# Kernel tuning notes

Measured on AMD Instinct MI355X. Metric: run time of the kernel, lower is better.

## Reference

```python
import jax, jax.numpy as jnp
import numpy as np

DIM, HEADS, WS = 192, 8, 8
B, H, W = 4, 256, 256


def conv2d(x, w, b=None, padding=((0, 0), (0, 0)), groups=1):
    y = jax.lax.conv_general_dilated(
        x, w, window_strides=(1, 1), padding=padding,
        dimension_numbers=("NCHW", "OIHW", "NCHW"), feature_group_count=groups)
    if b is not None:
        y = y + b[None, :, None, None]
    return y


def setup_inputs() -> dict:
    key = jax.random.key(0)
    ks = jax.random.split(key, 16)
    d = DIM
    s = 0.02
    return {
        "x": jax.random.normal(ks[0], (B, d, H, W), jnp.float32),
        "w_dww": jax.random.normal(ks[1], (d, 1, 1, 11), jnp.float32) * s,
        "b_dww": jnp.zeros((d,), jnp.float32),
        "w_dwh": jax.random.normal(ks[2], (d, 1, 11, 1), jnp.float32) * s,
        "b_dwh": jnp.zeros((d,), jnp.float32),
        "w_dwhw": jax.random.normal(ks[3], (2 * d, 1, 3, 3), jnp.float32) * s,
        "b_dwhw": jnp.zeros((2 * d,), jnp.float32),
        "w_conv1": jax.random.normal(ks[4], (d, 2 * d, 1, 1), jnp.float32) * s,
        "w_qkv": jax.random.normal(ks[5], (3 * d, d, 1, 1), jnp.float32) * s,
        "w_qkvdw": jax.random.normal(ks[6], (3 * d, 1, 3, 3), jnp.float32) * s,
        "w_conv2": jax.random.normal(ks[7], (d, d, 1, 1), jnp.float32) * s,
        "w_conv3": jax.random.normal(ks[8], (d, d, 1, 1), jnp.float32) * s,
        "w_conv4a": jax.random.normal(ks[9], (d, d, 1, 1), jnp.float32) * s,
        "w_conv4b": jax.random.normal(ks[10], (d, 1, 3, 3), jnp.float32) * s,
        "w_proj": jax.random.normal(ks[11], (d, 2 * d, 1, 1), jnp.float32) * s,
        "temperature": jnp.ones((HEADS, 1, 1), jnp.float32),
    }


def reference(x, w_dww, b_dww, w_dwh, b_dwh, w_dwhw, b_dwhw, w_conv1,
              w_qkv, w_qkvdw, w_conv2, w_conv3, w_conv4a, w_conv4b,
              w_proj, temperature):
    b, c, h, w = x.shape
    d, heads, ws = DIM, HEADS, WS

    # high-frequency branch: strip depthwise convs -> 3x3 depthwise -> 1x1
    hw_cat = jnp.concatenate([
        conv2d(x, w_dww, b_dww, padding=((0, 0), (5, 5)), groups=d),
        conv2d(x, w_dwh, b_dwh, padding=((5, 5), (0, 0)), groups=d)], axis=1)
    high = conv2d(hw_cat, w_dwhw, b_dwhw, padding=((1, 1), (1, 1)), groups=2 * d)
    high = conv2d(high, w_conv1)  # [b, d, h, w]

    # low-frequency branch: avg-pool downsample then channel attention
    x_down = x.reshape(b, c, h // ws, ws, w // ws, ws).mean(axis=(3, 5))
    qkv = conv2d(x_down, w_qkv)
    qkv = conv2d(qkv, w_qkvdw, padding=((1, 1), (1, 1)), groups=3 * d)
    q, k, v = jnp.split(qkv, 3, axis=1)

    hd, wd = h // ws, w // ws
    ch = d // heads
    q = q.reshape(b, heads, ch, hd * wd)
    k = k.reshape(b, heads, ch, hd * wd)
    q = q / jnp.maximum(jnp.linalg.norm(q, axis=-1, keepdims=True), 1e-12)
    k = k / jnp.maximum(jnp.linalg.norm(k, axis=-1, keepdims=True), 1e-12)
    attn = jnp.einsum("bhcn,bhdn->bhcd", q, k) * temperature[None]  # [b,heads,ch,ch]
    attn = jax.nn.softmax(attn, axis=-1)

    # pooling gate on v (global 1x1) then modulate full-res conv4(x)
    v_max = jnp.max(v, axis=(2, 3), keepdims=True)
    v_avg = jnp.mean(v, axis=(2, 3), keepdims=True)
    v_gate = conv2d(v_max, w_conv2) + conv2d(v_avg, w_conv3)  # [b, d, 1, 1]
    x4 = conv2d(conv2d(x, w_conv4a), w_conv4b, padding=((1, 1), (1, 1)), groups=d)
    v_full = v_gate * x4  # [b, d, h, w]

    v_full = v_full.reshape(b, heads, ch, h * w)
    low = jnp.einsum("bhcd,bhdn->bhcn", attn, v_full).reshape(b, d, h, w)

    return conv2d(jnp.concatenate([high, low], axis=1), w_proj)
```

## Files before the change

### kernel.cpp

```cpp
#include <hip/hip_runtime.h>
#include <hip/hip_bf16.h>

typedef __hip_bfloat16 bf16;
typedef __attribute__((ext_vector_type(8))) short s8v;
typedef __attribute__((ext_vector_type(4))) float f4;
typedef __attribute__((ext_vector_type(2))) float f2;

#define DEVI __device__ __forceinline__

DEVI f4 mfma16(s8v a, s8v b, f4 c){
  return __builtin_amdgcn_mfma_f32_16x16x32_bf16(a, b, c, 0, 0, 0);
}

constexpr int NPIX = 65536;
constexpr int NDOWN = 1024;

__global__ void k_cast_w(const float* __restrict__ w1, const float* __restrict__ w4a,
                         const float* __restrict__ wp, const float* __restrict__ wq,
                         bf16* __restrict__ out){
  int i = blockIdx.x*256 + threadIdx.x;
  if (i < 73728) out[i] = __float2bfloat16(w1[i]);
  else if (i < 110592) out[i] = __float2bfloat16(w4a[i - 73728]);
  else if (i < 184320) out[i] = __float2bfloat16(wp[i - 110592]);
  else if (i < 294912) out[i] = __float2bfloat16(wq[i - 184320]);
}

__global__ void k_pack_x(const float* __restrict__ x, bf16* __restrict__ xp){
  __shared__ float t[8][1032];
  int b = blockIdx.z, cb = blockIdx.y, ns = blockIdx.x, tid = threadIdx.x;
  const float* src = x + ((size_t)(b*192 + cb*8))*NPIX + ns*1024;
  #pragma unroll
  for (int i = 0; i < 8; ++i){
    float4 v = *(const float4*)(src + (size_t)i*NPIX + tid*4);
    *(float4*)&t[i][tid*4] = v;
  }
  __syncthreads();
  bf16* dst = xp + (((size_t)(b*24 + cb))*NPIX + ns*1024)*8;
  #pragma unroll
  for (int j = 0; j < 4; ++j){
    int p = j*256 + tid;
    alignas(16) bf16 c8[8];
    #pragma unroll
    for (int i = 0; i < 8; ++i) c8[i] = __float2bfloat16(t[i][p]);
    *(uint4*)(dst + (size_t)p*8) = *(const uint4*)c8;
  }
}

__global__ void k_pool(const bf16* __restrict__ xp, bf16* __restrict__ xdp){
  __shared__ float red[8][32][8];
  int b = blockIdx.z, cb = blockIdx.y, hd = blockIdx.x, tid = threadIdx.x;
  int r = tid >> 5, wd = tid & 31;
  const bf16* src = xp + (((size_t)(b*24 + cb))*NPIX + (hd*8 + r)*256 + wd*8)*8;
  float acc[8] = {0,0,0,0,0,0,0,0};
  #pragma unroll
  for (int ww = 0; ww < 8; ++ww){
    uint4 raw = *(const uint4*)(src + ww*8);
    const bf16* c8 = (const bf16*)&raw;
    #pragma unroll
    for (int i = 0; i < 8; ++i) acc[i] += __bfloat162float(c8[i]);
  }
  #pragma unroll
  for (int i = 0; i < 8; ++i) red[r][wd][i] = acc[i];
  __syncthreads();
  if (tid < 32){
    alignas(16) bf16 o8[8];
    #pragma unroll
    for (int i = 0; i < 8; ++i){
      float s = 0.f;
      #pragma unroll
      for (int rr = 0; rr < 8; ++rr) s += red[rr][tid][i];
      o8[i] = __float2bfloat16(s * (1.0f/64.0f));
    }
    *(uint4*)(xdp + (((size_t)(b*24 + cb))*NDOWN + hd*32 + tid)*8) = *(const uint4*)o8;
  }
}

template<int K, bool PLANAR>
__launch_bounds__(256, 2)
__global__ void k_gemm(const bf16* __restrict__ Bp, const bf16* __restrict__ W,
                       void* __restrict__ outp, int npix, int outkb){
  constexpr int KB8 = K/8;
  constexpr int NIT = K/64;
  __shared__ bf16 As[96*72];
  __shared__ bf16 Bs[128*72];
  int tid = threadIdx.x;
  int b = blockIdx.z;
  int m0 = blockIdx.y*96;
  int n0 = blockIdx.x*128;
  int wave = tid >> 6, lane = tid & 63;
  int wm = wave >> 1, wn = wave & 1;
  int lr = lane & 15, kg = lane >> 4;
  f4 acc[3][4] = {};
  const size_t bK = (size_t)b * KB8;
  for (int kt = 0; kt < NIT; ++kt){
    {
      int idx = tid;
      #pragma unroll
      for (int j = 0; j < 3; ++j, idx += 256){
        int m = idx >> 3, kc = idx & 7;
        *(uint4*)&As[m*72 + kc*8] = *(const uint4*)(W + (size_t)(m0 + m)*K + kt*64 + kc*8);
      }
      idx = tid;
      #pragma unroll
      for (int j = 0; j < 4; ++j, idx += 256){
        int kb = idx >> 7, n = idx & 127;
        *(uint4*)&Bs[n*72 + kb*8] = *(const uint4*)(Bp + ((bK + kt*8 + kb)*npix + n0 + n)*8);
      }
    }
    __syncthreads();
    #pragma unroll
    for (int kk = 0; kk < 2; ++kk){
      s8v af[3]; s8v bfr[4];
      int ko = kk*32 + kg*8;
      #pragma unroll
      for (int mf = 0; mf < 3; ++mf) af[mf] = *(const s8v*)&As[(wm*48 + mf*16 + lr)*72 + ko];
      #pragma unroll
      for (int nf = 0; nf < 4; ++nf) bfr[nf] = *(const s8v*)&Bs[(wn*64 + nf*16 + lr)*72 + ko];
      #pragma unroll
      for (int mf = 0; mf < 3; ++mf)
        #pragma unroll
        for (int nf = 0; nf < 4; ++nf)
          acc[mf][nf] = mfma16(af[mf], bfr[nf], acc[mf][nf]);
    }
    __syncthreads();
  }
  int quad = lane >> 4;
  #pragma unroll
  for (int mf = 0; mf < 3; ++mf){
    int mb = m0 + wm*48 + mf*16 + quad*4;
    #pragma unroll
    for (int nf = 0; nf < 4; ++nf){
      int n = n0 + wn*64 + nf*16 + lr;
      if constexpr (PLANAR){
        float* o = (float*)outp;
        #pragma unroll
        for (int r2 = 0; r2 < 4; ++r2)
          o[((size_t)(b*outkb + mb + r2))*npix + n] = acc[mf][nf][r2];
      } else {
        bf16* o = (bf16*)outp;
        alignas(8) bf16 v4[4];
        #pragma unroll
        for (int r2 = 0; r2 < 4; ++r2) v4[r2] = __float2bfloat16(acc[mf][nf][r2]);
        *(uint2*)(o + ((size_t)(b*outkb + (mb >> 3))*npix + n)*8 + (mb & 7)) = *(const uint2*)v4;
      }
    }
  }
}

__launch_bounds__(256, 4)
__global__ void k_high_dw(const bf16* __restrict__ xp,
    const float* __restrict__ wdww, const float* __restrict__ bdww,
    const float* __restrict__ wdwh, const float* __restrict__ bdwh,
    const float* __restrict__ w3, const float* __restrict__ b3,
    bf16* __restrict__ hw3p){
  __shared__ bf16 xs[28*29*8];
  __shared__ float dws[2*8*364];
  int t = blockIdx.x, cb = blockIdx.y, b = blockIdx.z, tid = threadIdx.x;
  int r0 = (t >> 4)*16, c0 = (t & 15)*16;

  const bf16* src = xp + ((size_t)(b*24 + cb))*NPIX*8;
  for (int i = tid; i < 784; i += 256){
    int r = i/28, c = i - r*28;
    int gr = r0 + r - 6, gc = c0 + c - 6;
    uint4 v = {0,0,0,0};
    if ((unsigned)gr < 256u && (unsigned)gc < 256u)
      v = *(const uint4*)(src + ((size_t)(gr*256 + gc))*8);
    *(uint4*)&xs[(r*29 + c)*8] = v;
  }
  __syncthreads();

  auto strip_task = [&](int task, bool isH){
    int ch = task & 7, idx = task >> 3;
    int cg = cb*8 + ch;
    const float* wsrc = isH ? (wdww + cg*11) : (wdwh + cg*11);
    float wv[11];
    #pragma unroll
    for (int j = 0; j < 11; ++j) wv[j] = wsrc[j];
    float bias = isH ? bdww[cg] : bdwh[cg];
    int base = isH ? ((idx + 5)*29)*8 + ch : (idx + 5)*8 + ch;
    int istr = isH ? 8 : 29*8;
    float vbuf[28];
    #pragma unroll
    for (int i = 0; i < 28; ++i)
      vbuf[i] = __bfloat162float(xs[base + i*istr]);
    int fixedv = (isH ? r0 : c0) + idx - 1;
    int varb   = (isH ? c0 : r0) - 1;
    bool fok = (unsigned)fixedv < 256u;
    float out[18];
    #pragma unroll
    for (int i = 0; i < 18; ++i){
      float s = bias;
      #pragma unroll
      for (int j = 0; j < 11; ++j) s += wv[j]*vbuf[i + j];
      bool ok = fok && ((unsigned)(varb + i) < 256u);
      out[i] = ok ? s : 0.f;
    }
    if (isH){
      float* ob = &dws[ch*364 + idx*20];
      #pragma unroll
      for (int q = 0; q < 4; ++q){
        f4 v; v[0] = out[q*4]; v[1] = out[q*4+1]; v[2] = out[q*4+2]; v[3] = out[q*4+3];
        *(f4*)(ob + q*4) = v;
      }
      f2 v2; v2[0] = out[16]; v2[1] = out[17];
      *(f2*)(ob + 16) = v2;
    } else {
      float* ob = &dws[(8 + ch)*364 + idx];
      #pragma unroll
      for (int i = 0; i < 18; ++i) ob[i*20] = out[i];
    }
  };
  {
    bool isH = tid < 144;
    int task = isH ? tid : tid - 144;
    strip_task(task, isH);
    if (tid >= 224) strip_task(tid - 112, false);
  }
  __syncthreads();

  {
    int branch = tid >> 7, rr = (tid >> 3) & 15, ch = tid & 7;
    int cg = cb*8 + ch;
    const float* wsrc = w3 + (branch*192 + cg)*9;
    float w[9];
    #pragma unroll
    for (int k = 0; k < 9; ++k) w[k] = wsrc[k];
    float bias = b3[branch*192 + cg];
    float acc[16];
    #pragma unroll
    for (int i = 0; i < 16; ++i) acc[i] = bias;
    const float* plane = &dws[(branch*8 + ch)*364];
    #pragma unroll
    for (int dr = 0; dr < 3; ++dr){
      const float* rp = plane + (rr + dr)*20;
      float rowv[18];
      #pragma unroll
      for (int q = 0; q < 4; ++q){
        f4 v = *(const f4*)(rp + q*4);
        rowv[q*4] = v[0]; rowv[q*4+1] = v[1]; rowv[q*4+2] = v[2]; rowv[q*4+3] = v[3];
      }
      {
        f2 v2 = *(const f2*)(rp + 16);
        rowv[16] = v2[0]; rowv[17] = v2[1];
      }
      #pragma unroll
      for (int dc = 0; dc < 3; ++dc){
        float wv = w[dr*3 + dc];
        #pragma unroll
        for (int i = 0; i < 16; ++i) acc[i] += wv * rowv[i + dc];
      }
    }
    bf16* o = hw3p + (((size_t)(b*48 + branch*24 + cb))*NPIX + (size_t)(r0 + rr)*256 + c0)*8 + ch;
    #pragma unroll
    for (int i = 0; i < 16; ++i) o[i*8] = __float2bfloat16(acc[i]);
  }
}

__global__ void k_qkv_dw(const bf16* __restrict__ qkv0p, const float* __restrict__ wdw,
                         float* __restrict__ qkvd, float* __restrict__ vmax, float* __restrict__ vavg){
  __shared__ bf16 xs[34*34*8];
  __shared__ float red[256*8];
  int cb = blockIdx.x, b = blockIdx.y, tid = threadIdx.x;
  for (int i = tid; i < 1156; i += 256){
    int r = i/34, c = i - r*34;
    int gr = r - 1, gc = c - 1;
    uint4 v = {0,0,0,0};
    if ((unsigned)gr < 32u && (unsigned)gc < 32u)
      v = *(const uint4*)(qkv0p + (((size_t)(b*72 + cb))*NDOWN + gr*32 + gc)*8);
    *(uint4*)&xs[i*8] = v;
  }
  __syncthreads();
  float mxv[8], smv[8];
  #pragma unroll
  for (int ch = 0; ch < 8; ++ch){ mxv[ch] = -3.4e38f; smv[ch] = 0.f; }
  for (int j = 0; j < 4; ++j){
    int p = j*256 + tid;
    int r = p >> 5, c = p & 31;
    #pragma unroll
    for (int ch = 0; ch < 8; ++ch){
      float s = 0.f;
      #pragma unroll
      for (int dr = 0; dr < 3; ++dr)
        #pragma unroll
        for (int dc = 0; dc < 3; ++dc)
          s += wdw[(cb*8 + ch)*9 + dr*3 + dc] *
               __bfloat162float(xs[((r + dr)*34 + c + dc)*8 + ch]);
      qkvd[((size_t)(b*576 + cb*8 + ch))*NDOWN + p] = s;
      mxv[ch] = fmaxf(mxv[ch], s);
      smv[ch] += s;
    }
  }
  if (cb >= 48){
    #pragma unroll
    for (int ch = 0; ch < 8; ++ch) red[tid*8 + ch] = mxv[ch];
    __syncthreads();
    for (int st = 128; st > 0; st >>= 1){
      if (tid < st)
        #pragma unroll
        for (int ch = 0; ch < 8; ++ch)
          red[tid*8 + ch] = fmaxf(red[tid*8 + ch], red[(tid + st)*8 + ch]);
      __syncthreads();
    }
    if (tid < 8) vmax[b*192 + (cb - 48)*8 + tid] = red[tid];
    __syncthreads();
    #pragma unroll
    for (int ch = 0; ch < 8; ++ch) red[tid*8 + ch] = smv[ch];
    __syncthreads();
    for (int st = 128; st > 0; st >>= 1){
      if (tid < st)
        #pragma unroll
        for (int ch = 0; ch < 8; ++ch) red[tid*8 + ch] += red[(tid + st)*8 + ch];
      __syncthreads();
    }
    if (tid < 8) vavg[b*192 + (cb - 48)*8 + tid] = red[tid] * (1.0f/1024.0f);
  }
}

__global__ void k_attn(const float* __restrict__ qkvd, const float* __restrict__ temp,
                       float* __restrict__ attn){
  __shared__ float inv[48];
  __shared__ float sm[576];
  int bh = blockIdx.x;
  int b = bh >> 3, h = bh & 7;
  const float* qb = qkvd + ((size_t)(b*576 + h*24))*NDOWN;
  const float* kb = qkvd + ((size_t)(b*576 + 192 + h*24))*NDOWN;
  int tid = threadIdx.x, wave = tid >> 6, lane = tid & 63;
  for (int v = wave; v < 48; v += 4){
    const float* p = (v < 24) ? (qb + v*NDOWN) : (kb + (v - 24)*NDOWN);
    float s = 0.f;
    for (int i = lane; i < NDOWN; i += 64){ float xv = p[i]; s += xv*xv; }
    #pragma unroll
    for (int o = 32; o > 0; o >>= 1) s += __shfl_down(s, o);
    if (lane == 0) inv[v] = 1.0f / fmaxf(sqrtf(s), 1e-12f);
  }
  __syncthreads();
  float tp = temp[h];
  for (int pr = tid; pr < 576; pr += 256){
    int c = pr/24, d = pr - c*24;
    const float4* qp = (const float4*)(qb + c*NDOWN);
    const float4* kp = (const float4*)(kb + d*NDOWN);
    float s = 0.f;
    for (int i = 0; i < 256; ++i){
      float4 a = qp[i], e = kp[i];
      s += a.x*e.x + a.y*e.y + a.z*e.z + a.w*e.w;
    }
    sm[pr] = s * inv[c] * inv[24 + d] * tp;
  }
  __syncthreads();
  if (tid < 24){
    float mx = -3.4e38f;
    for (int d = 0; d < 24; ++d) mx = fmaxf(mx, sm[tid*24 + d]);
    float sum = 0.f;
    for (int d = 0; d < 24; ++d) sum += __expf(sm[tid*24 + d] - mx);
    float isum = 1.0f / sum;
    for (int d = 0; d < 24; ++d)
      attn[((size_t)bh)*576 + tid*24 + d] = __expf(sm[tid*24 + d] - mx) * isum;
  }
}

__global__ void k_gate(const float* __restrict__ vmax, const float* __restrict__ vavg,
                       const float* __restrict__ w2, const float* __restrict__ w3,
                       float* __restrict__ gate){
  __shared__ float vm[192], va[192];
  int b = blockIdx.x, tid = threadIdx.x;
  if (tid < 192){ vm[tid] = vmax[b*192 + tid]; va[tid] = vavg[b*192 + tid]; }
  __syncthreads();
  if (tid < 192){
    float s = 0.f;
    const float* w2r = w2 + tid*192;
    const float* w3r = w3 + tid*192;
    for (int k = 0; k < 192; ++k) s += w2r[k]*vm[k] + w3r[k]*va[k];
    gate[b*192 + tid] = s;
  }
}

__global__ void k_low(const bf16* __restrict__ x4ap, const float* __restrict__ attn,
                      const float* __restrict__ gate, const float* __restrict__ w4b,
                      bf16* __restrict__ hlp){
  __shared__ bf16 xt[3*18*18*10];
  __shared__ float a2[576];
  __shared__ float wt[216];
  __shared__ float vt[24*256];
  int t = blockIdx.x, h = blockIdx.y, b = blockIdx.z, tid = threadIdx.x;
  int r0 = (t >> 4)*16, c0 = (t & 15)*16;
  int ch0 = h*24;
  for (int i = tid; i < 576; i += 256)
    a2[i] = attn[((size_t)(b*8 + h))*576 + i] * gate[b*192 + ch0 + (i % 24)];
  for (int i = tid; i < 216; i += 256) wt[i] = w4b[ch0*9 + i];
  for (int i = tid; i < 972; i += 256){
    int kb = i/324, p = i - kb*324;
    int r = p/18, c = p - r*18;
    int gr = r0 + r - 1, gc = c0 + c - 1;
    uint4 v = {0,0,0,0};
    if ((unsigned)gr < 256u && (unsigned)gc < 256u)
      v = *(const uint4*)(x4ap + (((size_t)(b*24 + h*3 + kb))*NPIX + gr*256 + gc)*8);
    const unsigned* u = (const unsigned*)&v;
    #pragma unroll
    for (int k = 0; k < 4; ++k) *(unsigned*)&xt[i*10 + k*2] = u[k];
  }
  __syncthreads();
  {
    int r = tid >> 4, c = tid & 15;
    #pragma unroll
    for (int ch = 0; ch < 24; ++ch){
      int kb = ch >> 3, ci = ch & 7;
      float s = 0.f;
      #pragma unroll
      for (int dr = 0; dr < 3; ++dr)
        #pragma unroll
        for (int dc = 0; dc < 3; ++dc)
          s += wt[ch*9 + dr*3 + dc] *
               __bfloat162float(xt[((kb*18 + r + dr)*18 + c + dc)*10 + ci]);
      vt[ch*256 + tid] = s;
    }
  }
  __syncthreads();
  {
    float o[24];
    #pragma unroll
    for (int cc = 0; cc < 24; ++cc){
      float s = 0.f;
      #pragma unroll
      for (int d = 0; d < 24; ++d) s += a2[cc*24 + d] * vt[d*256 + tid];
      o[cc] = s;
    }
    int n = (r0 + (tid >> 4))*256 + c0 + (tid & 15);
    #pragma unroll
    for (int kb = 0; kb < 3; ++kb){
      alignas(16) bf16 c8[8];
      #pragma unroll
      for (int i = 0; i < 8; ++i) c8[i] = __float2bfloat16(o[kb*8 + i]);
      *(uint4*)(hlp + (((size_t)(b*48 + 24 + h*3 + kb))*NPIX + n)*8) = *(const uint4*)c8;
    }
  }
}

extern "C" void kernel_launch(void* const* d_in, const int* in_sizes, int n_in,
                              void* d_out, int out_size, void* d_ws, size_t ws_size,
                              hipStream_t stream){
  const float* x        = (const float*)d_in[0];
  const float* w_dww    = (const float*)d_in[1];
  const float* b_dww    = (const float*)d_in[2];
  const float* w_dwh    = (const float*)d_in[3];
  const float* b_dwh    = (const float*)d_in[4];
  const float* w_dwhw   = (const float*)d_in[5];
  const float* b_dwhw   = (const float*)d_in[6];
  const float* w_conv1  = (const float*)d_in[7];
  const float* w_qkv    = (const float*)d_in[8];
  const float* w_qkvdw  = (const float*)d_in[9];
  const float* w_conv2  = (const float*)d_in[10];
  const float* w_conv3  = (const float*)d_in[11];
  const float* w_conv4a = (const float*)d_in[12];
  const float* w_conv4b = (const float*)d_in[13];
  const float* w_proj   = (const float*)d_in[14];
  const float* temp     = (const float*)d_in[15];

  char* ws = (char*)d_ws;
  size_t off = 0;
  auto take = [&](size_t bytes)->char*{
    char* r = ws + off;
    off = (off + bytes + 255) & ~(size_t)255;
    return r;
  };
  bf16*  xp    = (bf16*) take((size_t)4*192*65536*2);
  bf16*  hw3p  = (bf16*) take((size_t)4*384*65536*2);
  bf16*  hlp   = (bf16*) take((size_t)4*384*65536*2);
  bf16*  x4ap  = (bf16*) take((size_t)4*192*65536*2);
  bf16*  xdp   = (bf16*) take((size_t)4*192*1024*2);
  bf16*  qkv0p = (bf16*) take((size_t)4*576*1024*2);
  float* qkvd  = (float*)take((size_t)4*576*1024*4);
  float* attn  = (float*)take((size_t)4*8*576*4);
  float* vmax  = (float*)take((size_t)4*192*4);
  float* vavg  = (float*)take((size_t)4*192*4);
  float* gate  = (float*)take((size_t)4*192*4);
  bf16*  wbf   = (bf16*) take((size_t)294912*2);
  if (off > ws_size) return;

  k_cast_w<<<1152, 256, 0, stream>>>(w_conv1, w_conv4a, w_proj, w_qkv, wbf);
  k_pack_x<<<dim3(64,24,4), 256, 0, stream>>>(x, xp);
  k_pool<<<dim3(32,24,4), 256, 0, stream>>>(xp, xdp);
  k_gemm<192,false><<<dim3(8,6,4), 256, 0, stream>>>(xdp, wbf + 184320, qkv0p, 1024, 72);
  k_qkv_dw<<<dim3(72,4), 256, 0, stream>>>(qkv0p, w_qkvdw, qkvd, vmax, vavg);
  k_attn<<<32, 256, 0, stream>>>(qkvd, temp, attn);
  k_gate<<<4, 192, 0, stream>>>(vmax, vavg, w_conv2, w_conv3, gate);
  k_high_dw<<<dim3(256,24,4), 256, 0, stream>>>(xp, w_dww, b_dww, w_dwh, b_dwh, w_dwhw, b_dwhw, hw3p);
  k_gemm<384,false><<<dim3(512,2,4), 256, 0, stream>>>(hw3p, wbf, hlp, 65536, 48);
  k_gemm<192,false><<<dim3(512,2,4), 256, 0, stream>>>(xp, wbf + 73728, x4ap, 65536, 24);
  k_low<<<dim3(256,8,4), 256, 0, stream>>>(x4ap, attn, gate, w_conv4b, hlp);
  k_gemm<384,true><<<dim3(512,2,4), 256, 0, stream>>>(hlp, wbf + 110592, d_out, 65536, 192);
}
```

Measured before the change: 1.003 ms.

## Fold per-head attention and gate into per-batch projection weights

The per-pixel 24x24 attention mix and the gate multiply in the low branch are moved into the final projection weights. A small kernel builds per-batch effective weights W_proj_low·attn·diag(gate), and the final GEMM now takes a per-batch weight stride. The low-branch kernel becomes a plain 3x3 depthwise conv over 8-channel blocks, which removes the large per-pixel FMA work and the shared-memory staging. The cost is a per-batch weight buffer and one extra tiny kernel launch.

```diff
diff --git a/kernel.cpp b/kernel.cpp
--- a/kernel.cpp
+++ b/kernel.cpp
@@ -78,7 +78,7 @@
 template<int K, bool PLANAR>
 __launch_bounds__(256, 2)
 __global__ void k_gemm(const bf16* __restrict__ Bp, const bf16* __restrict__ W,
-                       void* __restrict__ outp, int npix, int outkb){
+                       void* __restrict__ outp, int npix, int outkb, unsigned wstride){
   constexpr int KB8 = K/8;
   constexpr int NIT = K/64;
   __shared__ bf16 As[96*72];
@@ -87,6 +87,7 @@
   int b = blockIdx.z;
   int m0 = blockIdx.y*96;
   int n0 = blockIdx.x*128;
+  W += (size_t)b * wstride;
   int wave = tid >> 6, lane = tid & 63;
   int wm = wave >> 1, wn = wave & 1;
   int lr = lane & 15, kg = lane >> 4;
@@ -374,64 +375,64 @@
   }
 }
 
-__global__ void k_low(const bf16* __restrict__ x4ap, const float* __restrict__ attn,
-                      const float* __restrict__ gate, const float* __restrict__ w4b,
-                      bf16* __restrict__ hlp){
-  __shared__ bf16 xt[3*18*18*10];
-  __shared__ float a2[576];
-  __shared__ float wt[216];
-  __shared__ float vt[24*256];
-  int t = blockIdx.x, h = blockIdx.y, b = blockIdx.z, tid = threadIdx.x;
+__global__ void k_weff(const float* __restrict__ attn, const float* __restrict__ gate,
+                       const float* __restrict__ wp, bf16* __restrict__ wfin){
+  __shared__ float A_s[576];
+  int bh = blockIdx.x; int b = bh >> 3, h = bh & 7;
+  int o = threadIdx.x;
+  for (int i = o; i < 576; i += 192) A_s[i] = attn[(size_t)bh*576 + i];
+  __syncthreads();
+  const float* wrow = wp + (size_t)o*384;
+  float wl[24];
+  #pragma unroll
+  for (int j = 0; j < 24; ++j) wl[j] = wrow[192 + h*24 + j];
+  bf16* dst = wfin + ((size_t)b*192 + o)*384;
+  #pragma unroll
+  for (int j = 0; j < 24; ++j) dst[h*24 + j] = __float2bfloat16(wrow[h*24 + j]);
+  #pragma unroll
+  for (int dl = 0; dl < 24; ++dl){
+    float s = 0.f;
+    #pragma unroll
+    for (int cl = 0; cl < 24; ++cl) s += wl[cl]*A_s[cl*24 + dl];
+    dst[192 + h*24 + dl] = __float2bfloat16(s * gate[b*192 + h*24 + dl]);
+  }
+}
+
+__global__ void k_x4(const bf16* __restrict__ x4ap, const float* __restrict__ w4b,
+                     bf16* __restrict__ hlp){
+  __shared__ bf16 xt[324*8];
+  __shared__ float wl4[72];
+  int t = blockIdx.x, cb = blockIdx.y, b = blockIdx.z, tid = threadIdx.x;
   int r0 = (t >> 4)*16, c0 = (t & 15)*16;
-  int ch0 = h*24;
-  for (int i = tid; i < 576; i += 256)
-    a2[i] = attn[((size_t)(b*8 + h))*576 + i] * gate[b*192 + ch0 + (i % 24)];
-  for (int i = tid; i < 216; i += 256) wt[i] = w4b[ch0*9 + i];
-  for (int i = tid; i < 972; i += 256){
-    int kb = i/324, p = i - kb*324;
-    int r = p/18, c = p - r*18;
+  if (tid < 72) wl4[tid] = w4b[cb*72 + tid];
+  for (int i = tid; i < 324; i += 256){
+    int r = i/18, c = i - r*18;
     int gr = r0 + r - 1, gc = c0 + c - 1;
     uint4 v = {0,0,0,0};
     if ((unsigned)gr < 256u && (unsigned)gc < 256u)
-      v = *(const uint4*)(x4ap + (((size_t)(b*24 + h*3 + kb))*NPIX + gr*256 + gc)*8);
-    const unsigned* u = (const unsigned*)&v;
-    #pragma unroll
-    for (int k = 0; k < 4; ++k) *(unsigned*)&xt[i*10 + k*2] = u[k];
+      v = *(const uint4*)(x4ap + (((size_t)(b*24 + cb))*NPIX + gr*256 + gc)*8);
+    *(uint4*)&xt[i*8] = v;
   }
   __syncthreads();
   {
     int r = tid >> 4, c = tid & 15;
-    #pragma unroll
-    for (int ch = 0; ch < 24; ++ch){
-      int kb = ch >> 3, ci = ch & 7;
-      float s = 0.f;
-      #pragma unroll
-      for (int dr = 0; dr < 3; ++dr)
-        #pragma unroll
-        for (int dc = 0; dc < 3; ++dc)
-          s += wt[ch*9 + dr*3 + dc] *
-               __bfloat162float(xt[((kb*18 + r + dr)*18 + c + dc)*10 + ci]);
-      vt[ch*256 + tid] = s;
-    }
-  }
-  __syncthreads();
-  {
-    float o[24];
-    #pragma unroll
-    for (int cc = 0; cc < 24; ++cc){
-      float s = 0.f;
-      #pragma unroll
-      for (int d = 0; d < 24; ++d) s += a2[cc*24 + d] * vt[d*256 + tid];
-      o[cc] = s;
-    }
-    int n = (r0 + (tid >> 4))*256 + c0 + (tid & 15);
-    #pragma unroll
-    for (int kb = 0; kb < 3; ++kb){
-      alignas(16) bf16 c8[8];
-      #pragma unroll
-      for (int i = 0; i < 8; ++i) c8[i] = __float2bfloat16(o[kb*8 + i]);
-      *(uint4*)(hlp + (((size_t)(b*48 + 24 + h*3 + kb))*NPIX + n)*8) = *(const uint4*)c8;
-    }
+    float acc[8] = {0,0,0,0,0,0,0,0};
+    #pragma unroll
+    for (int dr = 0; dr < 3; ++dr)
+      #pragma unroll
+      for (int dc = 0; dc < 3; ++dc){
+        uint4 v = *(const uint4*)&xt[((r + dr)*18 + c + dc)*8];
+        const bf16* c8 = (const bf16*)&v;
+        int tap = dr*3 + dc;
+        #pragma unroll
+        for (int ch = 0; ch < 8; ++ch)
+          acc[ch] += wl4[ch*9 + tap] * __bfloat162float(c8[ch]);
+      }
+    int n = (r0 + r)*256 + c0 + c;
+    alignas(16) bf16 o8[8];
+    #pragma unroll
+    for (int ch = 0; ch < 8; ++ch) o8[ch] = __float2bfloat16(acc[ch]);
+    *(uint4*)(hlp + (((size_t)(b*48 + 24 + cb))*NPIX + n)*8) = *(const uint4*)o8;
   }
 }
 
@@ -474,18 +475,20 @@
   float* vavg  = (float*)take((size_t)4*192*4);
   float* gate  = (float*)take((size_t)4*192*4);
   bf16*  wbf   = (bf16*) take((size_t)294912*2);
+  bf16*  wfin  = (bf16*) take((size_t)4*73728*2);
   if (off > ws_size) return;
 
   k_cast_w<<<1152, 256, 0, stream>>>(w_conv1, w_conv4a, w_proj, w_qkv, wbf);
   k_pack_x<<<dim3(64,24,4), 256, 0, stream>>>(x, xp);
   k_pool<<<dim3(32,24,4), 256, 0, stream>>>(xp, xdp);
-  k_gemm<192,false><<<dim3(8,6,4), 256, 0, stream>>>(xdp, wbf + 184320, qkv0p, 1024, 72);
+  k_gemm<192,false><<<dim3(8,6,4), 256, 0, stream>>>(xdp, wbf + 184320, qkv0p, 1024, 72, 0);
   k_qkv_dw<<<dim3(72,4), 256, 0, stream>>>(qkv0p, w_qkvdw, qkvd, vmax, vavg);
   k_attn<<<32, 256, 0, stream>>>(qkvd, temp, attn);
   k_gate<<<4, 192, 0, stream>>>(vmax, vavg, w_conv2, w_conv3, gate);
+  k_weff<<<32, 192, 0, stream>>>(attn, gate, w_proj, wfin);
   k_high_dw<<<dim3(256,24,4), 256, 0, stream>>>(xp, w_dww, b_dww, w_dwh, b_dwh, w_dwhw, b_dwhw, hw3p);
-  k_gemm<384,false><<<dim3(512,2,4), 256, 0, stream>>>(hw3p, wbf, hlp, 65536, 48);
-  k_gemm<192,false><<<dim3(512,2,4), 256, 0, stream>>>(xp, wbf + 73728, x4ap, 65536, 24);
-  k_low<<<dim3(256,8,4), 256, 0, stream>>>(x4ap, attn, gate, w_conv4b, hlp);
-  k_gemm<384,true><<<dim3(512,2,4), 256, 0, stream>>>(hlp, wbf + 110592, d_out, 65536, 192);
-}
+  k_gemm<384,false><<<dim3(512,2,4), 256, 0, stream>>>(hw3p, wbf, hlp, 65536, 48, 0);
+  k_gemm<192,false><<<dim3(512,2,4), 256, 0, stream>>>(xp, wbf + 73728, x4ap, 65536, 24, 0);
+  k_x4<<<dim3(256,24,4), 256, 0, stream>>>(x4ap, w_conv4b, hlp);
+  k_gemm<384,true><<<dim3(512,2,4), 256, 0, stream>>>(hlp, wfin, d_out, 65536, 192, 73728);
+}
```

New measurement: 922.9 us. 1.09x faster.
